# Performance work log

Hardware: AMD Instinct MI355X
Metric: run time of the kernel (lower is better)

## Reference

```python
import jax, jax.numpy as jnp
import numpy as np

B, D_IN, D_OUT = 8192, 1024, 1024


def setup_inputs() -> dict:
    key = jax.random.key(0)
    k1, k2 = jax.random.split(key)
    x = jax.random.normal(k1, (B, D_IN), dtype=jnp.float32)
    # Keras add_weight(shape=(3, input_dim, output_dim), initializer='uniform')
    kernel = jax.random.normal(k2, (3, D_IN, D_OUT), dtype=jnp.float32) * 0.05
    return {"x": x, "kernel": kernel}


def reference(x, kernel):
    # x: (B, D). Layer does expand_dims(axis=1) -> (B, 1, D) (seq_len == 1).
    output_dim = kernel.shape[-1]
    xe = x[:, None, :]                                   # (B, 1, D)
    q = jnp.einsum('bsd,do->bso', xe, kernel[0])         # (B, 1, O)
    k = jnp.einsum('bsd,do->bso', xe, kernel[1])         # (B, 1, O)
    v = jnp.einsum('bsd,do->bso', xe, kernel[2])         # (B, 1, O)
    scores = jnp.einsum('bqo,bko->bqk', q, k) / jnp.sqrt(
        jnp.asarray(output_dim, x.dtype))                # (B, 1, 1)
    attn = jax.nn.softmax(scores, axis=-1)
    out = jnp.einsum('bqk,bko->bqo', attn, v)            # (B, 1, O)
    return out
```

## Files before the change

kernel.cpp:

```cpp
#include <hip/hip_runtime.h>
#include <hip/hip_bf16.h>
#include <stdint.h>

#define AS1 __attribute__((address_space(1)))
#define AS3 __attribute__((address_space(3)))

typedef __attribute__((ext_vector_type(8))) short bf16x8_t;
typedef __attribute__((ext_vector_type(4))) float f32x4_t;

#define DDIM 1024
#define WT_ELEMS ((size_t)DDIM * DDIM)
#define XB_ELEMS ((size_t)8192 * DDIM)

static __device__ inline ushort f32_to_bf16_rne(float f) {
  union { float f; uint32_t u; } v;
  v.f = f;
  v.u += 0x7FFFu + ((v.u >> 16) & 1u);
  return (ushort)(v.u >> 16);
}

__global__ __launch_bounds__(256) void prep(const float* __restrict__ W,
                                            ushort* __restrict__ Wt,
                                            const float* __restrict__ X,
                                            ushort* __restrict__ Xb) {
  if (blockIdx.x < 256) {
    __shared__ float tile[64][65];
    const int t  = threadIdx.x;
    const int bk = blockIdx.x & 15;
    const int bn = blockIdx.x >> 4;
#pragma unroll
    for (int s = 0; s < 4; ++s) {
      const int slot = (s << 8) + t;
      const int r    = slot >> 4;
      const int c4   = (slot & 15) << 2;
      const float4 v = *(const float4*)(W + (size_t)(bk * 64 + r) * DDIM + bn * 64 + c4);
      tile[r][c4 + 0] = v.x; tile[r][c4 + 1] = v.y;
      tile[r][c4 + 2] = v.z; tile[r][c4 + 3] = v.w;
    }
    __syncthreads();
#pragma unroll
    for (int s = 0; s < 2; ++s) {
      const int slot = (s << 8) + t;
      const int n    = slot >> 3;
      const int k8   = (slot & 7) << 3;
      union { ushort h[8]; uint4 u; } tmp;
#pragma unroll
      for (int j = 0; j < 8; ++j) tmp.h[j] = f32_to_bf16_rne(tile[k8 + j][n]);
      *(uint4*)(Wt + (size_t)(bn * 64 + n) * DDIM + bk * 64 + k8) = tmp.u;
    }
  } else {
    const size_t i = ((size_t)(blockIdx.x - 256) * 256 + threadIdx.x) << 3;
    const float4 v0 = *(const float4*)(X + i);
    const float4 v1 = *(const float4*)(X + i + 4);
    union { ushort h[8]; uint4 u; } o;
    o.h[0] = f32_to_bf16_rne(v0.x); o.h[1] = f32_to_bf16_rne(v0.y);
    o.h[2] = f32_to_bf16_rne(v0.z); o.h[3] = f32_to_bf16_rne(v0.w);
    o.h[4] = f32_to_bf16_rne(v1.x); o.h[5] = f32_to_bf16_rne(v1.y);
    o.h[6] = f32_to_bf16_rne(v1.z); o.h[7] = f32_to_bf16_rne(v1.w);
    *(uint4*)(Xb + i) = o.u;
  }
}

__global__ __launch_bounds__(256, 2) void gemm_bb(const ushort* __restrict__ Xb,
                                                  const ushort* __restrict__ Wt,
                                                  float* __restrict__ C) {
  __shared__ __align__(16) ushort As[4][128 * 32];
  __shared__ __align__(16) ushort Bs[4][128 * 32];

  const int t    = threadIdx.x;
  const int wave = t >> 6;
  const int lane = t & 63;
  const int m0 = blockIdx.x * 128;
  const int n0 = blockIdx.y * 128;

  const int sr = t >> 2;
  const int sc = (t & 3) ^ ((sr >> 1) & 3);
  const ushort* aB = Xb + (size_t)(m0 + sr) * DDIM + (sc << 3);
  const ushort* bB = Wt + (size_t)(n0 + sr) * DDIM + (sc << 3);

  AS3 char* lA = (AS3 char*)&As[0][0];
  AS3 char* lB = (AS3 char*)&Bs[0][0];
  const int woff = wave << 10;

  const int wr = (wave >> 1) << 6;
  const int wc = (wave & 1) << 6;
  const int fr = lane & 15;
  const int fq = lane >> 4;

  f32x4_t acc[4][4] = {};

  auto issue = [&](int st) {
    const int p = st & 3;
    const ushort* a = aB + (st << 5);
    const ushort* b = bB + (st << 5);
    AS3 char* dA = lA + (p << 13) + woff;
    AS3 char* dB = lB + (p << 13) + woff;
#pragma unroll
    for (int j = 0; j < 2; ++j) {
      __builtin_amdgcn_global_load_lds((const AS1 void*)(a + (size_t)(j << 6) * DDIM),
                                       (AS3 void*)(dA + (j << 12)), 16, 0, 0);
      __builtin_amdgcn_global_load_lds((const AS1 void*)(b + (size_t)(j << 6) * DDIM),
                                       (AS3 void*)(dB + (j << 12)), 16, 0, 0);
    }
  };

  auto compute = [&](int p) {
    const ushort* Ab = &As[p][0];
    const ushort* Bb = &Bs[p][0];
    bf16x8_t af[4], bfr[4];
#pragma unroll
    for (int mi = 0; mi < 4; ++mi) {
      const int r = wr + (mi << 4) + fr;
      af[mi] = *(const bf16x8_t*)&Ab[(r << 5) + ((fq ^ ((r >> 1) & 3)) << 3)];
    }
#pragma unroll
    for (int ni = 0; ni < 4; ++ni) {
      const int r = wc + (ni << 4) + fr;
      bfr[ni] = *(const bf16x8_t*)&Bb[(r << 5) + ((fq ^ ((r >> 1) & 3)) << 3)];
    }
#pragma unroll
    for (int mi = 0; mi < 4; ++mi)
#pragma unroll
      for (int ni = 0; ni < 4; ++ni)
        acc[mi][ni] = __builtin_amdgcn_mfma_f32_16x16x32_bf16(af[mi], bfr[ni], acc[mi][ni], 0, 0, 0);
  };

  issue(0);
  issue(1);
  issue(2);
  asm volatile("s_waitcnt vmcnt(8)\n\ts_barrier" ::: "memory");

  for (int i = 0; i < 29; ++i) {
    issue(i + 3);
    asm volatile("s_waitcnt vmcnt(12)\n\ts_barrier" ::: "memory");
    compute(i & 3);
    asm volatile("s_barrier" ::: "memory");
  }
  asm volatile("s_waitcnt vmcnt(8)\n\ts_barrier" ::: "memory");
  compute(1);
  asm volatile("s_waitcnt vmcnt(4)\n\ts_barrier" ::: "memory");
  compute(2);
  asm volatile("s_waitcnt vmcnt(0)\n\ts_barrier" ::: "memory");
  compute(3);

#pragma unroll
  for (int mi = 0; mi < 4; ++mi) {
#pragma unroll
    for (int r = 0; r < 4; ++r) {
      const int row = m0 + wr + (mi << 4) + (fq << 2) + r;
      float* crow = C + (size_t)row * DDIM + n0 + wc + fr;
#pragma unroll
      for (int ni = 0; ni < 4; ++ni)
        crow[ni << 4] = acc[mi][ni][r];
    }
  }
}

__global__ __launch_bounds__(256) void gemm_xw(const float* __restrict__ X,
                                               const ushort* __restrict__ Wt,
                                               float* __restrict__ C) {
  __shared__ __align__(16) ushort As[128 * 32];
  __shared__ __align__(16) ushort Bs[128 * 32];
  const int t    = threadIdx.x;
  const int wave = t >> 6;
  const int lane = t & 63;
  const int m0 = blockIdx.x * 128;
  const int n0 = blockIdx.y * 128;
  const int srow  = (wave << 4) + (lane >> 2);
  const int skcol = (lane & 3) << 3;
  const ushort* bptr0 = Wt + (size_t)(n0 + srow) * DDIM + skcol;
  const ushort* bptr1 = Wt + (size_t)(n0 + 64 + srow) * DDIM + skcol;
  const int ar = t >> 2;
  const int ak = (t & 3) << 3;
  const float* aptr0 = X + (size_t)(m0 + ar) * DDIM + ak;
  const float* aptr1 = X + (size_t)(m0 + 64 + ar) * DDIM + ak;
  ushort* asw0 = &As[(ar << 5) + ak];
  ushort* asw1 = &As[((ar + 64) << 5) + ak];
  const int wr = (wave >> 1) << 6;
  const int wc = (wave & 1) << 6;
  const int fr = lane & 15;
  const int fq = lane >> 4;
  f32x4_t acc[4][4] = {};
  AS3 char* ldsB = (AS3 char*)Bs;
  const int woff = wave << 10;
  for (int kt = 0; kt < DDIM; kt += 32) {
    const float4 a00 = *(const float4*)(aptr0);
    const float4 a01 = *(const float4*)(aptr0 + 4);
    const float4 a10 = *(const float4*)(aptr1);
    const float4 a11 = *(const float4*)(aptr1 + 4);
    aptr0 += 32; aptr1 += 32;
    __syncthreads();
    __builtin_amdgcn_global_load_lds((const AS1 void*)bptr0, (AS3 void*)(ldsB + woff),        16, 0, 0);
    __builtin_amdgcn_global_load_lds((const AS1 void*)bptr1, (AS3 void*)(ldsB + 4096 + woff), 16, 0, 0);
    bptr0 += 32; bptr1 += 32;
    union { ushort h[8]; bf16x8_t v; } c0, c1;
    c0.h[0] = f32_to_bf16_rne(a00.x); c0.h[1] = f32_to_bf16_rne(a00.y);
    c0.h[2] = f32_to_bf16_rne(a00.z); c0.h[3] = f32_to_bf16_rne(a00.w);
    c0.h[4] = f32_to_bf16_rne(a01.x); c0.h[5] = f32_to_bf16_rne(a01.y);
    c0.h[6] = f32_to_bf16_rne(a01.z); c0.h[7] = f32_to_bf16_rne(a01.w);
    c1.h[0] = f32_to_bf16_rne(a10.x); c1.h[1] = f32_to_bf16_rne(a10.y);
    c1.h[2] = f32_to_bf16_rne(a10.z); c1.h[3] = f32_to_bf16_rne(a10.w);
    c1.h[4] = f32_to_bf16_rne(a11.x); c1.h[5] = f32_to_bf16_rne(a11.y);
    c1.h[6] = f32_to_bf16_rne(a11.z); c1.h[7] = f32_to_bf16_rne(a11.w);
    *(bf16x8_t*)asw0 = c0.v;
    *(bf16x8_t*)asw1 = c1.v;
    __syncthreads();
    bf16x8_t af[4], bfr[4];
#pragma unroll
    for (int mi = 0; mi < 4; ++mi)
      af[mi] = *(const bf16x8_t*)&As[((wr + (mi << 4) + fr) << 5) + (fq << 3)];
#pragma unroll
    for (int ni = 0; ni < 4; ++ni)
      bfr[ni] = *(const bf16x8_t*)&Bs[((wc + (ni << 4) + fr) << 5) + (fq << 3)];
#pragma unroll
    for (int mi = 0; mi < 4; ++mi)
#pragma unroll
      for (int ni = 0; ni < 4; ++ni)
        acc[mi][ni] = __builtin_amdgcn_mfma_f32_16x16x32_bf16(af[mi], bfr[ni], acc[mi][ni], 0, 0, 0);
  }
#pragma unroll
  for (int mi = 0; mi < 4; ++mi)
#pragma unroll
    for (int r = 0; r < 4; ++r) {
      const int row = m0 + wr + (mi << 4) + (fq << 2) + r;
      float* crow = C + (size_t)row * DDIM + n0 + wc + fr;
#pragma unroll
      for (int ni = 0; ni < 4; ++ni)
        crow[ni << 4] = acc[mi][ni][r];
    }
}

extern "C" void kernel_launch(void* const* d_in, const int* in_sizes, int n_in,
                              void* d_out, int out_size, void* d_ws, size_t ws_size,
                              hipStream_t stream) {
  const float* x    = (const float*)d_in[0];
  const float* kern = (const float*)d_in[1];
  const float* W = kern + (size_t)2 * DDIM * DDIM;
  ushort* Wt = (ushort*)d_ws;
  const int M = in_sizes[0] / DDIM;

  if (ws_size >= (WT_ELEMS + XB_ELEMS) * sizeof(ushort)) {
    ushort* Xb = (ushort*)d_ws + WT_ELEMS;
    const unsigned cvt_blocks = (unsigned)((size_t)M * DDIM / 8 / 256);
    prep<<<256 + cvt_blocks, 256, 0, stream>>>(W, Wt, x, Xb);
    gemm_bb<<<dim3(M / 128, DDIM / 128), 256, 0, stream>>>(Xb, Wt, (float*)d_out);
  } else {
    prep<<<256, 256, 0, stream>>>(W, Wt, x, (ushort*)nullptr);
    gemm_xw<<<dim3(M / 128, DDIM / 128), 256, 0, stream>>>(x, Wt, (float*)d_out);
  }
}
```

Before: 115.4 us.

## Shrink GEMM tile to 128x64 with double-buffered LDS for higher occupancy

Replaces the 128x128 tile, 4-stage LDS pipeline GEMM with a 128x64 tile and 2-stage double buffering. LDS use and accumulator registers per block drop, so launch bounds ask for 4 blocks per CU, and twice as many blocks are launched. The fallback fp32-input GEMM path is removed, so the workspace is now assumed large enough for the bf16 copy of X. In exchange, arithmetic intensity per block falls, A tiles are reloaded twice as often, and the pipeline prefetches only one stage ahead.

```diff
diff --git a/kernel.cpp b/kernel.cpp
--- a/kernel.cpp
+++ b/kernel.cpp
@@ -61,17 +61,17 @@
   }
 }
 
-__global__ __launch_bounds__(256, 2) void gemm_bb(const ushort* __restrict__ Xb,
+__global__ __launch_bounds__(256, 4) void gemm_d4(const ushort* __restrict__ Xb,
                                                   const ushort* __restrict__ Wt,
                                                   float* __restrict__ C) {
-  __shared__ __align__(16) ushort As[4][128 * 32];
-  __shared__ __align__(16) ushort Bs[4][128 * 32];
+  __shared__ __align__(16) ushort As[2][128 * 32];
+  __shared__ __align__(16) ushort Bs[2][64 * 32];
 
   const int t    = threadIdx.x;
   const int wave = t >> 6;
   const int lane = t & 63;
   const int m0 = blockIdx.x * 128;
-  const int n0 = blockIdx.y * 128;
+  const int n0 = blockIdx.y * 64;
 
   const int sr = t >> 2;
   const int sc = (t & 3) ^ ((sr >> 1) & 3);
@@ -83,65 +83,59 @@
   const int woff = wave << 10;
 
   const int wr = (wave >> 1) << 6;
-  const int wc = (wave & 1) << 6;
+  const int wc = (wave & 1) << 5;
   const int fr = lane & 15;
   const int fq = lane >> 4;
 
-  f32x4_t acc[4][4] = {};
+  f32x4_t acc[4][2] = {};
 
   auto issue = [&](int st) {
-    const int p = st & 3;
+    const int p = st & 1;
     const ushort* a = aB + (st << 5);
     const ushort* b = bB + (st << 5);
     AS3 char* dA = lA + (p << 13) + woff;
-    AS3 char* dB = lB + (p << 13) + woff;
+    AS3 char* dB = lB + (p << 12) + woff;
 #pragma unroll
     for (int j = 0; j < 2; ++j) {
       __builtin_amdgcn_global_load_lds((const AS1 void*)(a + (size_t)(j << 6) * DDIM),
                                        (AS3 void*)(dA + (j << 12)), 16, 0, 0);
-      __builtin_amdgcn_global_load_lds((const AS1 void*)(b + (size_t)(j << 6) * DDIM),
-                                       (AS3 void*)(dB + (j << 12)), 16, 0, 0);
     }
+    __builtin_amdgcn_global_load_lds((const AS1 void*)b, (AS3 void*)dB, 16, 0, 0);
   };
 
   auto compute = [&](int p) {
     const ushort* Ab = &As[p][0];
     const ushort* Bb = &Bs[p][0];
-    bf16x8_t af[4], bfr[4];
+    bf16x8_t af[4], bfr[2];
 #pragma unroll
     for (int mi = 0; mi < 4; ++mi) {
       const int r = wr + (mi << 4) + fr;
       af[mi] = *(const bf16x8_t*)&Ab[(r << 5) + ((fq ^ ((r >> 1) & 3)) << 3)];
     }
 #pragma unroll
-    for (int ni = 0; ni < 4; ++ni) {
+    for (int ni = 0; ni < 2; ++ni) {
       const int r = wc + (ni << 4) + fr;
       bfr[ni] = *(const bf16x8_t*)&Bb[(r << 5) + ((fq ^ ((r >> 1) & 3)) << 3)];
     }
 #pragma unroll
     for (int mi = 0; mi < 4; ++mi)
 #pragma unroll
-      for (int ni = 0; ni < 4; ++ni)
+      for (int ni = 0; ni < 2; ++ni)
         acc[mi][ni] = __builtin_amdgcn_mfma_f32_16x16x32_bf16(af[mi], bfr[ni], acc[mi][ni], 0, 0, 0);
   };
 
   issue(0);
-  issue(1);
-  issue(2);
-  asm volatile("s_waitcnt vmcnt(8)\n\ts_barrier" ::: "memory");
 
-  for (int i = 0; i < 29; ++i) {
-    issue(i + 3);
-    asm volatile("s_waitcnt vmcnt(12)\n\ts_barrier" ::: "memory");
-    compute(i & 3);
-    asm volatile("s_barrier" ::: "memory");
+  for (int i = 0; i < 32; ++i) {
+    if (i < 31) {
+      issue(i + 1);
+      asm volatile("s_waitcnt vmcnt(3)\n\ts_barrier" ::: "memory");
+    } else {
+      asm volatile("s_waitcnt vmcnt(0)\n\ts_barrier" ::: "memory");
+    }
+    compute(i & 1);
+    if (i < 31) asm volatile("s_barrier" ::: "memory");
   }
-  asm volatile("s_waitcnt vmcnt(8)\n\ts_barrier" ::: "memory");
-  compute(1);
-  asm volatile("s_waitcnt vmcnt(4)\n\ts_barrier" ::: "memory");
-  compute(2);
-  asm volatile("s_waitcnt vmcnt(0)\n\ts_barrier" ::: "memory");
-  compute(3);
 
 #pragma unroll
   for (int mi = 0; mi < 4; ++mi) {
@@ -150,84 +144,10 @@
       const int row = m0 + wr + (mi << 4) + (fq << 2) + r;
       float* crow = C + (size_t)row * DDIM + n0 + wc + fr;
 #pragma unroll
-      for (int ni = 0; ni < 4; ++ni)
+      for (int ni = 0; ni < 2; ++ni)
         crow[ni << 4] = acc[mi][ni][r];
     }
   }
-}
-
-__global__ __launch_bounds__(256) void gemm_xw(const float* __restrict__ X,
-                                               const ushort* __restrict__ Wt,
-                                               float* __restrict__ C) {
-  __shared__ __align__(16) ushort As[128 * 32];
-  __shared__ __align__(16) ushort Bs[128 * 32];
-  const int t    = threadIdx.x;
-  const int wave = t >> 6;
-  const int lane = t & 63;
-  const int m0 = blockIdx.x * 128;
-  const int n0 = blockIdx.y * 128;
-  const int srow  = (wave << 4) + (lane >> 2);
-  const int skcol = (lane & 3) << 3;
-  const ushort* bptr0 = Wt + (size_t)(n0 + srow) * DDIM + skcol;
-  const ushort* bptr1 = Wt + (size_t)(n0 + 64 + srow) * DDIM + skcol;
-  const int ar = t >> 2;
-  const int ak = (t & 3) << 3;
-  const float* aptr0 = X + (size_t)(m0 + ar) * DDIM + ak;
-  const float* aptr1 = X + (size_t)(m0 + 64 + ar) * DDIM + ak;
-  ushort* asw0 = &As[(ar << 5) + ak];
-  ushort* asw1 = &As[((ar + 64) << 5) + ak];
-  const int wr = (wave >> 1) << 6;
-  const int wc = (wave & 1) << 6;
-  const int fr = lane & 15;
-  const int fq = lane >> 4;
-  f32x4_t acc[4][4] = {};
-  AS3 char* ldsB = (AS3 char*)Bs;
-  const int woff = wave << 10;
-  for (int kt = 0; kt < DDIM; kt += 32) {
-    const float4 a00 = *(const float4*)(aptr0);
-    const float4 a01 = *(const float4*)(aptr0 + 4);
-    const float4 a10 = *(const float4*)(aptr1);
-    const float4 a11 = *(const float4*)(aptr1 + 4);
-    aptr0 += 32; aptr1 += 32;
-    __syncthreads();
-    __builtin_amdgcn_global_load_lds((const AS1 void*)bptr0, (AS3 void*)(ldsB + woff),        16, 0, 0);
-    __builtin_amdgcn_global_load_lds((const AS1 void*)bptr1, (AS3 void*)(ldsB + 4096 + woff), 16, 0, 0);
-    bptr0 += 32; bptr1 += 32;
-    union { ushort h[8]; bf16x8_t v; } c0, c1;
-    c0.h[0] = f32_to_bf16_rne(a00.x); c0.h[1] = f32_to_bf16_rne(a00.y);
-    c0.h[2] = f32_to_bf16_rne(a00.z); c0.h[3] = f32_to_bf16_rne(a00.w);
-    c0.h[4] = f32_to_bf16_rne(a01.x); c0.h[5] = f32_to_bf16_rne(a01.y);
-    c0.h[6] = f32_to_bf16_rne(a01.z); c0.h[7] = f32_to_bf16_rne(a01.w);
-    c1.h[0] = f32_to_bf16_rne(a10.x); c1.h[1] = f32_to_bf16_rne(a10.y);
-    c1.h[2] = f32_to_bf16_rne(a10.z); c1.h[3] = f32_to_bf16_rne(a10.w);
-    c1.h[4] = f32_to_bf16_rne(a11.x); c1.h[5] = f32_to_bf16_rne(a11.y);
-    c1.h[6] = f32_to_bf16_rne(a11.z); c1.h[7] = f32_to_bf16_rne(a11.w);
-    *(bf16x8_t*)asw0 = c0.v;
-    *(bf16x8_t*)asw1 = c1.v;
-    __syncthreads();
-    bf16x8_t af[4], bfr[4];
-#pragma unroll
-    for (int mi = 0; mi < 4; ++mi)
-      af[mi] = *(const bf16x8_t*)&As[((wr + (mi << 4) + fr) << 5) + (fq << 3)];
-#pragma unroll
-    for (int ni = 0; ni < 4; ++ni)
-      bfr[ni] = *(const bf16x8_t*)&Bs[((wc + (ni << 4) + fr) << 5) + (fq << 3)];
-#pragma unroll
-    for (int mi = 0; mi < 4; ++mi)
-#pragma unroll
-      for (int ni = 0; ni < 4; ++ni)
-        acc[mi][ni] = __builtin_amdgcn_mfma_f32_16x16x32_bf16(af[mi], bfr[ni], acc[mi][ni], 0, 0, 0);
-  }
-#pragma unroll
-  for (int mi = 0; mi < 4; ++mi)
-#pragma unroll
-    for (int r = 0; r < 4; ++r) {
-      const int row = m0 + wr + (mi << 4) + (fq << 2) + r;
-      float* crow = C + (size_t)row * DDIM + n0 + wc + fr;
-#pragma unroll
-      for (int ni = 0; ni < 4; ++ni)
-        crow[ni << 4] = acc[mi][ni][r];
-    }
 }
 
 extern "C" void kernel_launch(void* const* d_in, const int* in_sizes, int n_in,
@@ -237,15 +157,10 @@
   const float* kern = (const float*)d_in[1];
   const float* W = kern + (size_t)2 * DDIM * DDIM;
   ushort* Wt = (ushort*)d_ws;
+  ushort* Xb = (ushort*)d_ws + WT_ELEMS;
   const int M = in_sizes[0] / DDIM;
 
-  if (ws_size >= (WT_ELEMS + XB_ELEMS) * sizeof(ushort)) {
-    ushort* Xb = (ushort*)d_ws + WT_ELEMS;
-    const unsigned cvt_blocks = (unsigned)((size_t)M * DDIM / 8 / 256);
-    prep<<<256 + cvt_blocks, 256, 0, stream>>>(W, Wt, x, Xb);
-    gemm_bb<<<dim3(M / 128, DDIM / 128), 256, 0, stream>>>(Xb, Wt, (float*)d_out);
-  } else {
-    prep<<<256, 256, 0, stream>>>(W, Wt, x, (ushort*)nullptr);
-    gemm_xw<<<dim3(M / 128, DDIM / 128), 256, 0, stream>>>(x, Wt, (float*)d_out);
-  }
+  const unsigned cvt_blocks = (unsigned)((size_t)M * DDIM / 8 / 256);
+  prep<<<256 + cvt_blocks, 256, 0, stream>>>(W, Wt, x, Xb);
+  gemm_d4<<<dim3(M / 128, DDIM / 64), 256, 0, stream>>>(Xb, Wt, (float*)d_out);
 }
```

Measured after the change: 116.2 us. About the same (+0.7%).
